# Kernel tuning notes

Hardware: AMD Instinct MI355X
Metric: run time of the kernel (lower is better)

## Reference

```python
import jax, jax.numpy as jnp
import numpy as np

B, T, N1, N2, D, H, DH = 8, 4, 1024, 64, 1024, 16, 64
INNER = H * DH
EPS = 1e-5


def layernorm(x, g, b):
    mu = jnp.mean(x, axis=-1, keepdims=True)
    var = jnp.var(x, axis=-1, keepdims=True)
    return (x - mu) * jax.lax.rsqrt(var + EPS) * g + b


def setup_inputs() -> dict:
    key = jax.random.key(0)
    ks = jax.random.split(key, 8)
    s = 0.02
    return {
        "x": jax.random.normal(ks[0], (B, T, N1, D), jnp.float32),
        "latents": jax.random.normal(ks[1], (B, T, N2, D), jnp.float32),
        "gm": jnp.ones((D,), jnp.float32),
        "bm": jnp.zeros((D,), jnp.float32),
        "gl": jnp.ones((D,), jnp.float32),
        "bl": jnp.zeros((D,), jnp.float32),
        "Wq": jax.random.normal(ks[2], (D, INNER), jnp.float32) * s,
        "Wkv": jax.random.normal(ks[3], (D, 2 * INNER), jnp.float32) * s,
        "Wout": jax.random.normal(ks[4], (INNER, D), jnp.float32) * s,
        "Wd1": jax.random.normal(ks[5], (D, D // 4), jnp.float32) * s,
        "bd1": jnp.zeros((D // 4,), jnp.float32),
        "Wd2": jax.random.normal(ks[6], (D // 4, H), jnp.float32) * s,
        "bd2": jnp.zeros((H,), jnp.float32),
    }


def reference(x, latents, gm, bm, gl, bl, Wq, Wkv, Wout, Wd1, bd1, Wd2, bd2):
    b, t, n1, d = x.shape
    n2 = latents.shape[2]
    h, dh = H, DH
    scale = dh ** -0.5

    xn = layernorm(x, gm, bm)
    ln = layernorm(latents, gl, bl)

    # q: (b, h, t, n2, dh)
    q = (ln @ Wq).reshape(b, t, n2, h, dh).transpose(0, 3, 1, 2, 4)
    # kv over image tokens + first latent token -> nk = n1 + 1
    kv_in = jnp.concatenate([xn, ln[:, :, 0:1]], axis=2)
    nk = n1 + 1
    kv = (kv_in @ Wkv).reshape(b, t, nk, 2, h, dh)
    k = kv[:, :, :, 0].transpose(0, 3, 1, 2, 4)  # (b, h, t, nk, dh)
    v = kv[:, :, :, 1].transpose(0, 3, 1, 2, 4)

    sim = jnp.einsum('bhtid,bhtjd->bhtij', q * scale, k)
    sim = sim - jax.lax.stop_gradient(jnp.max(sim, axis=-1, keepdims=True))
    attn = jax.nn.softmax(sim, axis=-1)

    # dynamic per-head weights from mean-pooled (normed) latents: (b, t, h)
    hid = jax.nn.relu(ln.mean(axis=2) @ Wd1 + bd1)
    dw = jax.nn.softmax(hid @ Wd2 + bd2, axis=-1)
    attn = attn * dw.transpose(0, 2, 1)[:, :, :, None, None]  # (b,h,t,1,1)

    out = jnp.einsum('bhtij,bhtjd->bhtid', attn, v)
    out = out.transpose(0, 2, 3, 1, 4).reshape(b, t, n2, h * dh)
    return out @ Wout
```

## Files before the change

### kernel.cpp

```cpp
#include <hip/hip_runtime.h>
#include <cstdint>
#include <cstddef>

constexpr int CB = 8, CT = 4, CN1 = 1024, CN2 = 64, CD = 1024, CH = 16, CDH = 64;
constexpr int CBT = CB * CT;
constexpr int CNK = CN1 + 1;
constexpr int CINNER = CH * CDH;

__device__ __forceinline__ unsigned short f2bf(float f) {
  union { float f; unsigned int u; } v; v.f = f;
  unsigned int u = v.u;
  u += 0x7fffu + ((u >> 16) & 1u);
  return (unsigned short)(u >> 16);
}

typedef __attribute__((ext_vector_type(8))) short short8;
typedef __attribute__((ext_vector_type(8))) __bf16 bf16x8;
typedef __attribute__((ext_vector_type(4))) float floatx4;

template <typename V>
__device__ __forceinline__ auto mfma_bf16_impl(V a, V b, floatx4 c, int)
    -> decltype(__builtin_amdgcn_mfma_f32_16x16x32_bf16(a, b, c, 0, 0, 0)) {
  return __builtin_amdgcn_mfma_f32_16x16x32_bf16(a, b, c, 0, 0, 0);
}
template <typename V>
__device__ __forceinline__ floatx4 mfma_bf16_impl(V a, V b, floatx4 c, long) {
  return __builtin_amdgcn_mfma_f32_16x16x32_bf16(
      __builtin_bit_cast(bf16x8, a), __builtin_bit_cast(bf16x8, b), c, 0, 0, 0);
}
__device__ __forceinline__ floatx4 mfma_bf16(short8 a, short8 b, floatx4 c) {
  return mfma_bf16_impl(a, b, c, 0);
}

#if __has_builtin(__builtin_amdgcn_global_load_lds)
#define HAS_GLDS 1
__device__ __forceinline__ void glds16(const unsigned short* g, unsigned short* l) {
  __builtin_amdgcn_global_load_lds(
      (const __attribute__((address_space(1))) void*)g,
      (__attribute__((address_space(3))) void*)l, 16, 0, 0);
}
#else
#define HAS_GLDS 0
#endif

__global__ __launch_bounds__(256) void ln_kernel(
    const float* __restrict__ x, const float* __restrict__ g,
    const float* __restrict__ b, unsigned short* __restrict__ obf,
    float* __restrict__ of32) {
  const int row = blockIdx.x * 4 + (threadIdx.x >> 6);
  const int lane = threadIdx.x & 63;
  const float4* xr = (const float4*)(x + (size_t)row * CD);
  float4 v[4];
#pragma unroll
  for (int k = 0; k < 4; ++k) v[k] = xr[lane + 64 * k];
  float s = 0.f, s2 = 0.f;
#pragma unroll
  for (int k = 0; k < 4; ++k) {
    s  += v[k].x + v[k].y + v[k].z + v[k].w;
    s2 += v[k].x*v[k].x + v[k].y*v[k].y + v[k].z*v[k].z + v[k].w*v[k].w;
  }
#pragma unroll
  for (int off = 32; off; off >>= 1) { s += __shfl_xor(s, off); s2 += __shfl_xor(s2, off); }
  const float mean = s * (1.0f / 1024.0f);
  const float var  = s2 * (1.0f / 1024.0f) - mean * mean;
  const float rstd = rsqrtf(var + 1e-5f);
#pragma unroll
  for (int k = 0; k < 4; ++k) {
    const float4 gv = ((const float4*)g)[lane + 64 * k];
    const float4 bv = ((const float4*)b)[lane + 64 * k];
    float4 y;
    y.x = (v[k].x - mean) * rstd * gv.x + bv.x;
    y.y = (v[k].y - mean) * rstd * gv.y + bv.y;
    y.z = (v[k].z - mean) * rstd * gv.z + bv.z;
    y.w = (v[k].w - mean) * rstd * gv.w + bv.w;
    ushort4 o; o.x = f2bf(y.x); o.y = f2bf(y.y); o.z = f2bf(y.z); o.w = f2bf(y.w);
    ((ushort4*)(obf + (size_t)row * CD))[lane + 64 * k] = o;
    if (of32) ((float4*)(of32 + (size_t)row * CD))[lane + 64 * k] = y;
  }
}

__global__ __launch_bounds__(256) void wtrans_kernel(
    const float* __restrict__ W, unsigned short* __restrict__ WT, int K, int N) {
  __shared__ float t[64][65];
  const int n0 = blockIdx.x * 64, k0 = blockIdx.y * 64;
  const int tid = threadIdx.x;
  const int kr = tid >> 4, ns = (tid & 15) * 4;
#pragma unroll
  for (int i = 0; i < 4; ++i) {
    const int k = kr + i * 16;
    const float4 v = *(const float4*)&W[(size_t)(k0 + k) * N + n0 + ns];
    t[k][ns + 0] = v.x; t[k][ns + 1] = v.y; t[k][ns + 2] = v.z; t[k][ns + 3] = v.w;
  }
  __syncthreads();
  const int n = tid >> 2, ks = (tid & 3) * 16;
#pragma unroll
  for (int c = 0; c < 4; ++c) {
    ushort4 o;
    o.x = f2bf(t[ks + c * 4 + 0][n]);
    o.y = f2bf(t[ks + c * 4 + 1][n]);
    o.z = f2bf(t[ks + c * 4 + 2][n]);
    o.w = f2bf(t[ks + c * 4 + 3][n]);
    *(ushort4*)&WT[(size_t)(n0 + n) * K + k0 + ks + c * 4] = o;
  }
}

template <bool A_KV, bool C_BF16>
__global__ __launch_bounds__(256) void gemm128_kernel(
    const unsigned short* __restrict__ A, const unsigned short* __restrict__ xn,
    const unsigned short* __restrict__ lnb, const unsigned short* __restrict__ BT,
    unsigned short* __restrict__ Cb, float* __restrict__ Cf,
    int M, int N, int K) {
  __shared__ __attribute__((aligned(16))) unsigned short As[128 * 32];
  __shared__ __attribute__((aligned(16))) unsigned short Bs[128 * 32];
  const int tid = threadIdx.x;
  const int col0 = blockIdx.x * 128, row0 = blockIdx.y * 128;
  const int srow = tid >> 2, skseg = (tid & 3) * 8;

  auto arow_ptr = [&](int grow) -> const unsigned short* {
    if (grow >= M) grow = M - 1;
    if (A_KV) {
      const int bt = grow / CNK, j = grow - bt * CNK;
      return (j < CN1) ? xn + ((size_t)(bt * CN1 + j)) * K + skseg
                       : lnb + ((size_t)(bt * CN2)) * K + skseg;
    }
    return A + (size_t)grow * K + skseg;
  };
  const unsigned short* a0 = arow_ptr(row0 + srow);
  const unsigned short* a1 = arow_ptr(row0 + 64 + srow);
  const unsigned short* b0 = BT + (size_t)(col0 + srow) * K + skseg;
  const unsigned short* b1 = BT + (size_t)(col0 + 64 + srow) * K + skseg;

  const int lane = tid & 63, wave = tid >> 6;
  const int wrow = (wave >> 1) * 64, wcol = (wave & 1) * 64;
  const int i16 = lane & 15, quad = lane >> 4;

  floatx4 acc[4][4] = {};
  for (int kt = 0; kt < K; kt += 32) {
    __syncthreads();
#if HAS_GLDS
    glds16(a0 + kt, &As[tid * 8]);
    glds16(a1 + kt, &As[2048 + tid * 8]);
    glds16(b0 + kt, &Bs[tid * 8]);
    glds16(b1 + kt, &Bs[2048 + tid * 8]);
#else
    *(uint4*)&As[tid * 8]        = *(const uint4*)(a0 + kt);
    *(uint4*)&As[2048 + tid * 8] = *(const uint4*)(a1 + kt);
    *(uint4*)&Bs[tid * 8]        = *(const uint4*)(b0 + kt);
    *(uint4*)&Bs[2048 + tid * 8] = *(const uint4*)(b1 + kt);
#endif
    __syncthreads();
    short8 af[4], bf[4];
#pragma unroll
    for (int ti = 0; ti < 4; ++ti)
      af[ti] = *(const short8*)&As[(wrow + ti * 16 + i16) * 32 + quad * 8];
#pragma unroll
    for (int tj = 0; tj < 4; ++tj)
      bf[tj] = *(const short8*)&Bs[(wcol + tj * 16 + i16) * 32 + quad * 8];
#pragma unroll
    for (int ti = 0; ti < 4; ++ti)
#pragma unroll
      for (int tj = 0; tj < 4; ++tj)
        acc[ti][tj] = mfma_bf16(af[ti], bf[tj], acc[ti][tj]);
  }
#pragma unroll
  for (int ti = 0; ti < 4; ++ti)
#pragma unroll
    for (int tj = 0; tj < 4; ++tj) {
      const int gc = col0 + wcol + tj * 16 + i16;
#pragma unroll
      for (int r = 0; r < 4; ++r) {
        const int gr = row0 + wrow + ti * 16 + quad * 4 + r;
        if (gr < M) {
          if (C_BF16) Cb[(size_t)gr * N + gc] = f2bf(acc[ti][tj][r]);
          else        Cf[(size_t)gr * N + gc] = acc[ti][tj][r];
        }
      }
    }
}

template <bool A_KV>
__global__ __launch_bounds__(256) void gemmkv_kernel(
    const unsigned short* __restrict__ xn, const unsigned short* __restrict__ lnb,
    const unsigned short* __restrict__ BT, unsigned short* __restrict__ Cb,
    int M, int N, int K, int nbN) {
  __shared__ __attribute__((aligned(16))) unsigned short As[3 * 4096];
  __shared__ __attribute__((aligned(16))) unsigned short Bs[3 * 4096];
  const int tid = threadIdx.x;

  const int raw = blockIdx.x;
  const int cpx = gridDim.x >> 3;
  const int virt = (raw & 7) * cpx + (raw >> 3);
  const int mb = virt / nbN, nb = virt - mb * nbN;
  const int row0 = mb * 128, col0 = nb * 128;

  auto arow = [&](int grow) -> const unsigned short* {
    if (grow >= M) grow = M - 1;
    if (A_KV) {
      const int bt = grow / CNK, j = grow - bt * CNK;
      return (j < CN1) ? xn + ((size_t)(bt * CN1 + j)) * K
                       : lnb + ((size_t)(bt * CN2)) * K;
    }
    return (const unsigned short*)nullptr;
  };
  const int c0 = tid, c1 = tid + 256;
  const int rA0 = c0 >> 2, sA0 = (c0 & 3) ^ ((rA0 >> 1) & 3);
  const int rA1 = c1 >> 2, sA1 = (c1 & 3) ^ ((rA1 >> 1) & 3);
  const unsigned short* pA0 = arow(row0 + rA0) + sA0 * 8;
  const unsigned short* pA1 = arow(row0 + rA1) + sA1 * 8;
  const unsigned short* pB0 = BT + (size_t)(col0 + rA0) * K + sA0 * 8;
  const unsigned short* pB1 = BT + (size_t)(col0 + rA1) * K + sA1 * 8;

  auto stage = [&](int s) {
    const int sb = (s % 3) * 4096;
#if HAS_GLDS
    glds16(pA0 + s * 32, &As[sb + tid * 8]);
    glds16(pA1 + s * 32, &As[sb + 2048 + tid * 8]);
    glds16(pB0 + s * 32, &Bs[sb + tid * 8]);
    glds16(pB1 + s * 32, &Bs[sb + 2048 + tid * 8]);
#else
    *(uint4*)&As[sb + tid * 8]        = *(const uint4*)(pA0 + s * 32);
    *(uint4*)&As[sb + 2048 + tid * 8] = *(const uint4*)(pA1 + s * 32);
    *(uint4*)&Bs[sb + tid * 8]        = *(const uint4*)(pB0 + s * 32);
    *(uint4*)&Bs[sb + 2048 + tid * 8] = *(const uint4*)(pB1 + s * 32);
#endif
  };

  const int lane = tid & 63, wave = tid >> 6;
  const int wr = wave >> 1, wc = wave & 1;
  const int i16 = lane & 15, quad = lane >> 4;
  int offA[4], offB[4];
#pragma unroll
  for (int ti = 0; ti < 4; ++ti) {
    const int r = wr * 64 + ti * 16 + i16;
    offA[ti] = r * 32 + (quad ^ ((r >> 1) & 3)) * 8;
  }
#pragma unroll
  for (int tj = 0; tj < 4; ++tj) {
    const int r = wc * 64 + tj * 16 + i16;
    offB[tj] = r * 32 + (quad ^ ((r >> 1) & 3)) * 8;
  }

  floatx4 acc[4][4] = {};
  const int NSL = K >> 5;
  stage(0); stage(1);

  auto phase = [&](int s, bool do_stage) {
    const unsigned short* Asl = &As[(s % 3) * 4096];
    const unsigned short* Bsl = &Bs[(s % 3) * 4096];
    short8 bf[4], af[4];
#pragma unroll
    for (int tj = 0; tj < 4; ++tj) bf[tj] = *(const short8*)(Bsl + offB[tj]);
#pragma unroll
    for (int ti = 0; ti < 4; ++ti) af[ti] = *(const short8*)(Asl + offA[ti]);
    if (do_stage) stage(s + 2);
    __builtin_amdgcn_s_setprio(1);
#pragma unroll
    for (int ti = 0; ti < 4; ++ti)
#pragma unroll
      for (int tj = 0; tj < 4; ++tj)
        acc[ti][tj] = mfma_bf16(af[ti], bf[tj], acc[ti][tj]);
    __builtin_amdgcn_s_setprio(0);
  };

  for (int s = 0; s < NSL - 2; ++s) {
    asm volatile("s_waitcnt vmcnt(4)" ::: "memory");
    __builtin_amdgcn_s_barrier();
    __builtin_amdgcn_sched_barrier(0);
    phase(s, true);
  }
  asm volatile("s_waitcnt vmcnt(4)" ::: "memory");
  __builtin_amdgcn_s_barrier();
  __builtin_amdgcn_sched_barrier(0);
  phase(NSL - 2, false);
  asm volatile("s_waitcnt vmcnt(0)" ::: "memory");
  __builtin_amdgcn_s_barrier();
  __builtin_amdgcn_sched_barrier(0);
  phase(NSL - 1, false);

#pragma unroll
  for (int ti = 0; ti < 4; ++ti)
#pragma unroll
    for (int tj = 0; tj < 4; ++tj) {
      const int gc = col0 + wc * 64 + tj * 16 + i16;
#pragma unroll
      for (int r = 0; r < 4; ++r) {
        const int gr = row0 + wr * 64 + ti * 16 + quad * 4 + r;
        if (gr < M) Cb[(size_t)gr * N + gc] = f2bf(acc[ti][tj][r]);
      }
    }
}

__global__ __launch_bounds__(256) void dwmean_kernel(
    const float* __restrict__ lnf, float* __restrict__ meanp) {
  const int bt = blockIdx.x >> 2, dseg = blockIdx.x & 3;
  const int d = dseg * 256 + threadIdx.x;
  const float* base = lnf + (size_t)bt * CN2 * CD + d;
  float s = 0.f;
#pragma unroll 4
  for (int r = 0; r < CN2; ++r) s += base[(size_t)r * CD];
  meanp[bt * CD + d] = s * (1.0f / 64.0f);
}

__global__ __launch_bounds__(256) void dwmlp_kernel(
    const float* __restrict__ meanp, const float* __restrict__ Wd1,
    const float* __restrict__ bd1, float* __restrict__ hidp) {
  __shared__ float red[8][32];
  const int bt = blockIdx.x >> 3, og = blockIdx.x & 7;
  const int o = threadIdx.x & 31, seg = threadIdx.x >> 5;
  const int col = og * 32 + o;
  const float* mb = meanp + bt * CD;
  float s = 0.f;
#pragma unroll 4
  for (int d = seg * 128; d < seg * 128 + 128; ++d)
    s += mb[d] * Wd1[(size_t)d * 256 + col];
  red[seg][o] = s;
  __syncthreads();
  if (seg == 0) {
    float t = red[0][o];
#pragma unroll
    for (int k = 1; k < 8; ++k) t += red[k][o];
    hidp[bt * 256 + col] = fmaxf(t + bd1[col], 0.0f);
  }
}

__global__ __launch_bounds__(256) void dwfin_kernel(
    const float* __restrict__ hidp, const float* __restrict__ Wd2,
    const float* __restrict__ bd2, float* __restrict__ dw) {
  __shared__ float red[16][16];
  __shared__ float lg[16];
  const int bt = blockIdx.x;
  const int h = threadIdx.x & 15, seg = threadIdx.x >> 4;
  const float* hb = hidp + bt * 256;
  float s = 0.f;
#pragma unroll
  for (int o = seg * 16; o < seg * 16 + 16; ++o)
    s += hb[o] * Wd2[o * 16 + h];
  red[seg][h] = s;
  __syncthreads();
  if (seg == 0) {
    float t = red[0][h];
#pragma unroll
    for (int k = 1; k < 16; ++k) t += red[k][h];
    lg[h] = t + bd2[h];
  }
  __syncthreads();
  if (threadIdx.x < 16) {
    float mx = lg[0];
#pragma unroll
    for (int k = 1; k < 16; ++k) mx = fmaxf(mx, lg[k]);
    float sum = 0.f;
#pragma unroll
    for (int k = 0; k < 16; ++k) sum += __expf(lg[k] - mx);
    dw[bt * 16 + threadIdx.x] = __expf(lg[threadIdx.x] - mx) / sum;
  }
}

__global__ __launch_bounds__(256) void attn_kernel(
    const unsigned short* __restrict__ Q,
    const unsigned short* __restrict__ KV,
    const float* __restrict__ dw,
    unsigned short* __restrict__ AO) {
  __shared__ __attribute__((aligned(16))) unsigned short ks[2][64 * 72];
  __shared__ __attribute__((aligned(16))) unsigned short vt[2][64 * 72];
  const int raw = blockIdx.x;
  const int bt = (raw & 7) * 4 + ((raw >> 3) >> 4);
  const int h  = (raw >> 3) & 15;
  const int tid = threadIdx.x;
  const int lane = tid & 63, wave = tid >> 6;
  const int i16 = lane & 15, quad = lane >> 4;
  const int wrow = wave * 16;

  const unsigned short* qbase =
      Q + ((size_t)(bt * 64 + wrow + i16)) * CINNER + h * 64;
  const short8 bq0 = *(const short8*)(qbase + quad * 8);
  const short8 bq1 = *(const short8*)(qbase + 32 + quad * 8);

  const int jrb = tid & 31, seg = tid >> 5;
  const int t_ = jrb & 15, hlf_ = jrb >> 4;
  const int vcol0 = ((t_ >> 2) << 3) + (t_ & 3) + 4 * hlf_;
  const unsigned short* kvb = KV + ((size_t)bt * CNK) * 2048 + h * 64 + seg * 8;

  uint4 kk[2], vv[2];
  auto load_tile = [&](int j0) {
#pragma unroll
    for (int c = 0; c < 2; ++c) {
      const int j = j0 + c * 32 + jrb;
      if (j < CNK) {
        const unsigned short* p = kvb + (size_t)j * 2048;
        kk[c] = *(const uint4*)p;
        vv[c] = *(const uint4*)(p + 1024);
      } else {
        kk[c] = make_uint4(0, 0, 0, 0);
        vv[c] = make_uint4(0, 0, 0, 0);
      }
    }
  };
  auto write_tile = [&](int buf) {
#pragma unroll
    for (int c = 0; c < 2; ++c) {
      const int jr = c * 32 + jrb;
      *(uint4*)&ks[buf][jr * 72 + seg * 8] = kk[c];
      const int vcol = c * 32 + vcol0;
      const unsigned int w[4] = {vv[c].x, vv[c].y, vv[c].z, vv[c].w};
#pragma unroll
      for (int p = 0; p < 4; ++p) {
        vt[buf][(seg * 8 + 2 * p + 0) * 72 + vcol] = (unsigned short)(w[p] & 0xffffu);
        vt[buf][(seg * 8 + 2 * p + 1) * 72 + vcol] = (unsigned short)(w[p] >> 16);
      }
    }
  };

  float l = 0.f;
  floatx4 O[4] = {{0,0,0,0}, {0,0,0,0}, {0,0,0,0}, {0,0,0,0}};
  const float expC = 0.18033688011112042f;

  load_tile(0);
  write_tile(0);
  constexpr int NT = 17;
  for (int t = 0; t < NT; ++t) {
    if (t + 1 < NT) load_tile((t + 1) * 64);
    __syncthreads();
    const int buf = t & 1;
    const unsigned short* ksb = ks[buf];
    const unsigned short* vtb = vt[buf];
#pragma unroll
    for (int c = 0; c < 2; ++c) {
      floatx4 s0 = {0,0,0,0}, s1 = {0,0,0,0};
      const short8 a00 = *(const short8*)&ksb[((2*c)   * 16 + i16) * 72 + quad * 8];
      const short8 a01 = *(const short8*)&ksb[((2*c)   * 16 + i16) * 72 + 32 + quad * 8];
      const short8 a10 = *(const short8*)&ksb[((2*c+1) * 16 + i16) * 72 + quad * 8];
      const short8 a11 = *(const short8*)&ksb[((2*c+1) * 16 + i16) * 72 + 32 + quad * 8];
      s0 = mfma_bf16(a00, bq0, s0); s0 = mfma_bf16(a01, bq1, s0);
      s1 = mfma_bf16(a10, bq0, s1); s1 = mfma_bf16(a11, bq1, s1);
      unsigned short pb0[4], pb1[4];
      if (t == NT - 1) {
#pragma unroll
        for (int r = 0; r < 4; ++r) {
          const int k0g = t * 64 + (2*c)   * 16 + quad * 4 + r;
          const int k1g = t * 64 + (2*c+1) * 16 + quad * 4 + r;
          const float p0 = (k0g < CNK) ? exp2f(s0[r] * expC) : 0.f;
          const float p1 = (k1g < CNK) ? exp2f(s1[r] * expC) : 0.f;
          l += p0 + p1;
          pb0[r] = f2bf(p0); pb1[r] = f2bf(p1);
        }
      } else {
#pragma unroll
        for (int r = 0; r < 4; ++r) {
          const float p0 = exp2f(s0[r] * expC);
          const float p1 = exp2f(s1[r] * expC);
          l += p0 + p1;
          pb0[r] = f2bf(p0); pb1[r] = f2bf(p1);
        }
      }
      const short8 bp = {
          (short)pb0[0], (short)pb0[1], (short)pb0[2], (short)pb0[3],
          (short)pb1[0], (short)pb1[1], (short)pb1[2], (short)pb1[3]};
#pragma unroll
      for (int dt = 0; dt < 4; ++dt) {
        const short8 av = *(const short8*)&vtb[(dt * 16 + i16) * 72 + c * 32 + quad * 8];
        O[dt] = mfma_bf16(av, bp, O[dt]);
      }
    }
    if (t + 1 < NT) write_tile((t + 1) & 1);
  }

  l += __shfl_xor(l, 16);
  l += __shfl_xor(l, 32);
  const float wsc = dw[bt * 16 + h] / l;
  unsigned short* obase = AO + ((size_t)(bt * 64 + wrow + i16)) * CINNER + h * 64;
#pragma unroll
  for (int dt = 0; dt < 4; ++dt)
#pragma unroll
    for (int r = 0; r < 4; ++r)
      obase[dt * 16 + quad * 4 + r] = f2bf(O[dt][r] * wsc);
}

extern "C" void kernel_launch(void* const* d_in, const int* in_sizes, int n_in,
                              void* d_out, int out_size, void* d_ws, size_t ws_size,
                              hipStream_t stream) {
  const float* x       = (const float*)d_in[0];
  const float* latents = (const float*)d_in[1];
  const float* gm  = (const float*)d_in[2];
  const float* bm  = (const float*)d_in[3];
  const float* gl  = (const float*)d_in[4];
  const float* bl  = (const float*)d_in[5];
  const float* Wq  = (const float*)d_in[6];
  const float* Wkv = (const float*)d_in[7];
  const float* Wout= (const float*)d_in[8];
  const float* Wd1 = (const float*)d_in[9];
  const float* bd1 = (const float*)d_in[10];
  const float* Wd2 = (const float*)d_in[11];
  const float* bd2 = (const float*)d_in[12];
  float* out = (float*)d_out;

  char* ws = (char*)d_ws;
  size_t off = 0;
  auto alloc = [&](size_t bytes) -> void* {
    void* p = ws + off;
    off += (bytes + 255) & ~(size_t)255;
    return p;
  };
  unsigned short* xn   = (unsigned short*)alloc((size_t)CBT * CN1 * CD * 2);
  unsigned short* kv   = (unsigned short*)alloc((size_t)CBT * CNK * 2048 * 2);
  float*          lnf  = (float*)        alloc((size_t)CBT * CN2 * CD * 4);
  unsigned short* lnb  = (unsigned short*)alloc((size_t)CBT * CN2 * CD * 2);
  unsigned short* wqT  = (unsigned short*)alloc((size_t)CD * CINNER * 2);
  unsigned short* wkvT = (unsigned short*)alloc((size_t)CD * 2 * CINNER * 2);
  unsigned short* woT  = (unsigned short*)alloc((size_t)CINNER * CD * 2);
  unsigned short* qb   = (unsigned short*)alloc((size_t)CBT * CN2 * CINNER * 2);
  unsigned short* aob  = (unsigned short*)alloc((size_t)CBT * CN2 * CINNER * 2);
  float*          dwp  = (float*)        alloc((size_t)CBT * CH * 4);
  float*          meanp= (float*)        alloc((size_t)CBT * CD * 4);
  float*          hidp = (float*)        alloc((size_t)CBT * 256 * 4);
  if (off > ws_size) return;

  ln_kernel<<<CBT * CN1 / 4, 256, 0, stream>>>(x, gm, bm, xn, nullptr);
  ln_kernel<<<CBT * CN2 / 4, 256, 0, stream>>>(latents, gl, bl, lnb, lnf);
  wtrans_kernel<<<dim3(CINNER / 64, CD / 64), 256, 0, stream>>>(Wq, wqT, CD, CINNER);
  wtrans_kernel<<<dim3(2 * CINNER / 64, CD / 64), 256, 0, stream>>>(Wkv, wkvT, CD, 2 * CINNER);
  wtrans_kernel<<<dim3(CD / 64, CINNER / 64), 256, 0, stream>>>(Wout, woT, CINNER, CD);
  gemm128_kernel<false, true><<<dim3(1024 / 128, 2048 / 128), 256, 0, stream>>>(
      lnb, nullptr, nullptr, wqT, qb, nullptr, 2048, 1024, 1024);
  {
    const int MB = (CBT * CNK + 127) / 128;
    gemmkv_kernel<true><<<MB * 16, 256, 0, stream>>>(
        xn, lnb, wkvT, kv, CBT * CNK, 2048, 1024, 16);
  }
  dwmean_kernel<<<CBT * 4, 256, 0, stream>>>(lnf, meanp);
  dwmlp_kernel<<<CBT * 8, 256, 0, stream>>>(meanp, Wd1, bd1, hidp);
  dwfin_kernel<<<CBT, 256, 0, stream>>>(hidp, Wd2, bd2, dwp);
  attn_kernel<<<CBT * CH, 256, 0, stream>>>(qb, kv, dwp, aob);
  gemm128_kernel<false, false><<<dim3(1024 / 128, 2048 / 128), 256, 0, stream>>>(
      aob, nullptr, nullptr, woT, nullptr, out, 2048, 1024, 1024);
}
```

Baseline: 529.8 us.

## Enlarge KV GEMM tile to 256x256 and read B fragments directly from global

The KV projection GEMM now uses 512-thread blocks computing 256x256 output tiles, with each wave owning a 128x64 sub-tile, which raises arithmetic intensity per staged A tile. Only A is staged through LDS in a triple buffer. B fragments are loaded straight from global memory into registers with a register double buffer, removing the LDS traffic and space B used before. The grid swizzle is dropped in favour of plain row-major block mapping. This raises register pressure (32 accumulators per wave) and depends on B reads being served well from cache, since they are no longer shared through LDS.

```diff
diff --git a/kernel.cpp b/kernel.cpp
--- a/kernel.cpp
+++ b/kernel.cpp
@@ -179,19 +179,14 @@
 }
 
 template <bool A_KV>
-__global__ __launch_bounds__(256) void gemmkv_kernel(
+__global__ __launch_bounds__(512, 2) void gemmkv_kernel(
     const unsigned short* __restrict__ xn, const unsigned short* __restrict__ lnb,
     const unsigned short* __restrict__ BT, unsigned short* __restrict__ Cb,
-    int M, int N, int K, int nbN) {
-  __shared__ __attribute__((aligned(16))) unsigned short As[3 * 4096];
-  __shared__ __attribute__((aligned(16))) unsigned short Bs[3 * 4096];
+    int M, int N, int K) {
+  __shared__ __attribute__((aligned(16))) unsigned short As[3 * 8192];
   const int tid = threadIdx.x;
-
-  const int raw = blockIdx.x;
-  const int cpx = gridDim.x >> 3;
-  const int virt = (raw & 7) * cpx + (raw >> 3);
-  const int mb = virt / nbN, nb = virt - mb * nbN;
-  const int row0 = mb * 128, col0 = nb * 128;
+  const int mb = blockIdx.x >> 3, nb = blockIdx.x & 7;
+  const int row0 = mb * 256, col0 = nb * 256;
 
   auto arow = [&](int grow) -> const unsigned short* {
     if (grow >= M) grow = M - 1;
@@ -202,89 +197,91 @@
     }
     return (const unsigned short*)nullptr;
   };
-  const int c0 = tid, c1 = tid + 256;
+  const int c0 = tid, c1 = tid + 512;
   const int rA0 = c0 >> 2, sA0 = (c0 & 3) ^ ((rA0 >> 1) & 3);
   const int rA1 = c1 >> 2, sA1 = (c1 & 3) ^ ((rA1 >> 1) & 3);
   const unsigned short* pA0 = arow(row0 + rA0) + sA0 * 8;
   const unsigned short* pA1 = arow(row0 + rA1) + sA1 * 8;
-  const unsigned short* pB0 = BT + (size_t)(col0 + rA0) * K + sA0 * 8;
-  const unsigned short* pB1 = BT + (size_t)(col0 + rA1) * K + sA1 * 8;
 
   auto stage = [&](int s) {
-    const int sb = (s % 3) * 4096;
+    const int sb = (s % 3) * 8192;
 #if HAS_GLDS
     glds16(pA0 + s * 32, &As[sb + tid * 8]);
-    glds16(pA1 + s * 32, &As[sb + 2048 + tid * 8]);
-    glds16(pB0 + s * 32, &Bs[sb + tid * 8]);
-    glds16(pB1 + s * 32, &Bs[sb + 2048 + tid * 8]);
+    glds16(pA1 + s * 32, &As[sb + 4096 + tid * 8]);
 #else
     *(uint4*)&As[sb + tid * 8]        = *(const uint4*)(pA0 + s * 32);
-    *(uint4*)&As[sb + 2048 + tid * 8] = *(const uint4*)(pA1 + s * 32);
-    *(uint4*)&Bs[sb + tid * 8]        = *(const uint4*)(pB0 + s * 32);
-    *(uint4*)&Bs[sb + 2048 + tid * 8] = *(const uint4*)(pB1 + s * 32);
+    *(uint4*)&As[sb + 4096 + tid * 8] = *(const uint4*)(pA1 + s * 32);
 #endif
   };
 
   const int lane = tid & 63, wave = tid >> 6;
-  const int wr = wave >> 1, wc = wave & 1;
+  const int wr = wave >> 2, wc = wave & 3;
   const int i16 = lane & 15, quad = lane >> 4;
-  int offA[4], offB[4];
-#pragma unroll
-  for (int ti = 0; ti < 4; ++ti) {
-    const int r = wr * 64 + ti * 16 + i16;
+  int offA[8];
+#pragma unroll
+  for (int ti = 0; ti < 8; ++ti) {
+    const int r = wr * 128 + ti * 16 + i16;
     offA[ti] = r * 32 + (quad ^ ((r >> 1) & 3)) * 8;
   }
+  const unsigned short* pB[4];
 #pragma unroll
   for (int tj = 0; tj < 4; ++tj) {
-    const int r = wc * 64 + tj * 16 + i16;
-    offB[tj] = r * 32 + (quad ^ ((r >> 1) & 3)) * 8;
-  }
-
-  floatx4 acc[4][4] = {};
+    const int col = col0 + wc * 64 + tj * 16 + i16;
+    pB[tj] = BT + (size_t)col * K + quad * 8;
+  }
+
+  floatx4 acc[8][4] = {};
+  short8 bfA[4], bfB[4];
+
+  stage(0); stage(1);
+  __builtin_amdgcn_sched_barrier(0);
+#pragma unroll
+  for (int tj = 0; tj < 4; ++tj) bfA[tj] = *(const short8*)(pB[tj]);
+  __builtin_amdgcn_sched_barrier(0);
+
+  auto phase = [&](int s, short8 (&bfC)[4], short8 (&bfN)[4], bool preB, bool doStage) {
+    const unsigned short* Asl = &As[(s % 3) * 8192];
+    if (preB) {
+#pragma unroll
+      for (int tj = 0; tj < 4; ++tj)
+        bfN[tj] = *(const short8*)(pB[tj] + (s + 1) * 32);
+    }
+    __builtin_amdgcn_sched_barrier(0);
+    short8 af[8];
+#pragma unroll
+    for (int ti = 0; ti < 8; ++ti) af[ti] = *(const short8*)(Asl + offA[ti]);
+    if (doStage) stage(s + 2);
+    __builtin_amdgcn_sched_barrier(0);
+    __builtin_amdgcn_s_setprio(1);
+#pragma unroll
+    for (int ti = 0; ti < 8; ++ti)
+#pragma unroll
+      for (int tj = 0; tj < 4; ++tj)
+        acc[ti][tj] = mfma_bf16(af[ti], bfC[tj], acc[ti][tj]);
+    __builtin_amdgcn_s_setprio(0);
+  };
+
   const int NSL = K >> 5;
-  stage(0); stage(1);
-
-  auto phase = [&](int s, bool do_stage) {
-    const unsigned short* Asl = &As[(s % 3) * 4096];
-    const unsigned short* Bsl = &Bs[(s % 3) * 4096];
-    short8 bf[4], af[4];
-#pragma unroll
-    for (int tj = 0; tj < 4; ++tj) bf[tj] = *(const short8*)(Bsl + offB[tj]);
-#pragma unroll
-    for (int ti = 0; ti < 4; ++ti) af[ti] = *(const short8*)(Asl + offA[ti]);
-    if (do_stage) stage(s + 2);
-    __builtin_amdgcn_s_setprio(1);
-#pragma unroll
-    for (int ti = 0; ti < 4; ++ti)
-#pragma unroll
-      for (int tj = 0; tj < 4; ++tj)
-        acc[ti][tj] = mfma_bf16(af[ti], bf[tj], acc[ti][tj]);
-    __builtin_amdgcn_s_setprio(0);
-  };
-
-  for (int s = 0; s < NSL - 2; ++s) {
-    asm volatile("s_waitcnt vmcnt(4)" ::: "memory");
+  for (int s = 0; s < NSL; s += 2) {
+    asm volatile("s_waitcnt vmcnt(6)" ::: "memory");
     __builtin_amdgcn_s_barrier();
     __builtin_amdgcn_sched_barrier(0);
-    phase(s, true);
-  }
-  asm volatile("s_waitcnt vmcnt(4)" ::: "memory");
-  __builtin_amdgcn_s_barrier();
-  __builtin_amdgcn_sched_barrier(0);
-  phase(NSL - 2, false);
-  asm volatile("s_waitcnt vmcnt(0)" ::: "memory");
-  __builtin_amdgcn_s_barrier();
-  __builtin_amdgcn_sched_barrier(0);
-  phase(NSL - 1, false);
-
-#pragma unroll
-  for (int ti = 0; ti < 4; ++ti)
+    phase(s, bfA, bfB, true, s + 2 < NSL);
+    if (s + 1 == NSL - 1) { asm volatile("s_waitcnt vmcnt(4)" ::: "memory"); }
+    else                  { asm volatile("s_waitcnt vmcnt(6)" ::: "memory"); }
+    __builtin_amdgcn_s_barrier();
+    __builtin_amdgcn_sched_barrier(0);
+    phase(s + 1, bfB, bfA, s + 2 < NSL, s + 3 < NSL);
+  }
+
+#pragma unroll
+  for (int ti = 0; ti < 8; ++ti)
 #pragma unroll
     for (int tj = 0; tj < 4; ++tj) {
       const int gc = col0 + wc * 64 + tj * 16 + i16;
 #pragma unroll
       for (int r = 0; r < 4; ++r) {
-        const int gr = row0 + wr * 64 + ti * 16 + quad * 4 + r;
+        const int gr = row0 + wr * 128 + ti * 16 + quad * 4 + r;
         if (gr < M) Cb[(size_t)gr * N + gc] = f2bf(acc[ti][tj][r]);
       }
     }
@@ -522,9 +519,9 @@
   gemm128_kernel<false, true><<<dim3(1024 / 128, 2048 / 128), 256, 0, stream>>>(
       lnb, nullptr, nullptr, wqT, qb, nullptr, 2048, 1024, 1024);
   {
-    const int MB = (CBT * CNK + 127) / 128;
-    gemmkv_kernel<true><<<MB * 16, 256, 0, stream>>>(
-        xn, lnb, wkvT, kv, CBT * CNK, 2048, 1024, 16);
+    const int MB = (CBT * CNK + 255) / 256;
+    gemmkv_kernel<true><<<MB * 8, 512, 0, stream>>>(
+        xn, lnb, wkvT, kv, CBT * CNK, 2048, 1024);
   }
   dwmean_kernel<<<CBT * 4, 256, 0, stream>>>(lnf, meanp);
   dwmlp_kernel<<<CBT * 8, 256, 0, stream>>>(meanp, Wd1, bd1, hidp);
```

Measured after the change: 602.4 us. 13.7% more time.
